# Kernel tuning notes

Hardware: AMD Instinct MI355X
Metric: run time of the kernel (lower is better)

## Reference

```python
import jax, jax.numpy as jnp
import numpy as np

T, N, C, D, S = 512, 32, 1296, 512, 30
NORM_SCALE = 32.0
NEGINF = -1e9


def setup_inputs() -> dict:
    key = jax.random.key(0)
    k1, k2, k3, k4, k5 = jax.random.split(key, 5)
    feats = jax.random.normal(k1, (T * N, D), dtype=jnp.float32)
    classifier_weight = jax.random.normal(k2, (D, C), dtype=jnp.float32)
    labeling = jax.random.randint(k3, (N, S), 1, C)  # targets cannot be blank(0)
    logit_lgts = (T - jax.random.randint(k4, (N,), 0, 32)).astype(jnp.int32)
    labeling_lgts = (S - jax.random.randint(k5, (N,), 0, 5)).astype(jnp.int32)
    return dict(feats=feats, classifier_weight=classifier_weight,
                labeling=labeling, logit_lgts=logit_lgts, labeling_lgts=labeling_lgts)


def _ctc_loss(log_probs, labels, in_lens, lab_lens):
    # log_probs: (T, N, C); labels: (N, S); blank = 0; reduction = 'sum'
    Tt, Nn, Cc = log_probs.shape
    Ss = labels.shape[1]
    L = 2 * Ss + 1
    # extended labeling: blank, l1, blank, l2, ..., blank  -> (N, L)
    ext = jnp.zeros((Nn, L), dtype=labels.dtype).at[:, 1::2].set(labels)
    # gather per-state log-probs: (T, N, L)
    lp_ext = jnp.take_along_axis(log_probs, jnp.broadcast_to(ext[None], (Tt, Nn, L)), axis=2)
    # skip transition s-2 -> s allowed iff s > 1 and ext[s] != ext[s-2]
    skip_ok = jnp.concatenate(
        [jnp.zeros((Nn, 2), dtype=bool), ext[:, 2:] != ext[:, :-2]], axis=1)
    alpha0 = (jnp.full((Nn, L), NEGINF, dtype=log_probs.dtype)
              .at[:, 0].set(lp_ext[0, :, 0])
              .at[:, 1].set(lp_ext[0, :, 1]))

    def step(alpha, inp):
        lp_t, t = inp  # lp_t: (N, L)
        a1 = alpha
        a2 = jnp.pad(alpha[:, :-1], ((0, 0), (1, 0)), constant_values=NEGINF)
        a3 = jnp.where(skip_ok,
                       jnp.pad(alpha[:, :-2], ((0, 0), (2, 0)), constant_values=NEGINF),
                       NEGINF)
        new = jax.nn.logsumexp(jnp.stack([a1, a2, a3], axis=0), axis=0) + lp_t
        # freeze alpha once t reaches a sample's input length
        alpha = jnp.where((t < in_lens)[:, None], new, alpha)
        return alpha, None

    alpha, _ = jax.lax.scan(step, alpha0, (lp_ext[1:], jnp.arange(1, Tt)))
    Ln = 2 * lab_lens + 1  # (N,)
    last = jnp.take_along_axis(alpha, (Ln - 1)[:, None], axis=1)[:, 0]
    last2 = jnp.take_along_axis(alpha, (Ln - 2)[:, None], axis=1)[:, 0]
    nll = -jnp.logaddexp(last, last2)
    return jnp.sum(nll)


def reference(feats, classifier_weight, labeling, logit_lgts, labeling_lgts):
    # RadialCTC: cosine logits with norm_scale, then CTC on log-softmax.
    w_n = classifier_weight / jnp.linalg.norm(classifier_weight, axis=0, keepdims=True)  # (D, C)
    f_n = feats / jnp.linalg.norm(feats, axis=1, keepdims=True)  # (T*N, D)
    logits = NORM_SCALE * (f_n @ w_n)  # (T*N, C)
    log_probs = jax.nn.log_softmax(logits.reshape(T, N, C), axis=-1)
    return _ctc_loss(log_probs, labeling, logit_lgts, labeling_lgts)
```

## Files before the change

### kernel.cpp

```cpp
#include <hip/hip_runtime.h>
#include <stdint.h>
#include <stddef.h>


typedef _Float16 f16;
typedef _Float16 f16x8 __attribute__((ext_vector_type(8)));
typedef float f32x4 __attribute__((ext_vector_type(4)));
typedef __attribute__((address_space(1))) void* as1_void_ptr;
typedef __attribute__((address_space(3))) void* as3_void_ptr;

#define TT 512
#define NN 32
#define CC 1296
#define DD 512
#define SS 30
#define CP 1408
#define LL 61
#define NORM_SCALE 32.0f
#define LOG2E 1.4426950408889634f
#define LN2   0.6931471805599453f

#define PREP_WBLK (CP / 16)
#define PREP_ZBLK 16
#define PREP_FBLK (TT * NN / 4)

#define GEMM_BLK ((TT * NN / 128) * (CP / 128))
#define MEGA_GC  NN
#define MEGA_BLK (MEGA_GC + GEMM_BLK)

__device__ __forceinline__ float fexp2(float x) { return __builtin_amdgcn_exp2f(x); }
__device__ __forceinline__ float flog2(float x) { return __builtin_amdgcn_logf(x); }

__device__ __forceinline__ double dpp_sr1_zero64(double x) {
    long long b = __double_as_longlong(x);
    int lo = (int)(b & 0xFFFFFFFFLL);
    int hi = (int)(b >> 32);
    int lo2 = __builtin_amdgcn_update_dpp(0, lo, 0x138, 0xF, 0xF, false);
    int hi2 = __builtin_amdgcn_update_dpp(0, hi, 0x138, 0xF, 0xF, false);
    return __longlong_as_double(((long long)hi2 << 32) |
                                (unsigned long long)(unsigned int)lo2);
}
__device__ __forceinline__ double dpp_sl1_zero64(double x) {
    long long b = __double_as_longlong(x);
    int lo = (int)(b & 0xFFFFFFFFLL);
    int hi = (int)(b >> 32);
    int lo2 = __builtin_amdgcn_update_dpp(0, lo, 0x130, 0xF, 0xF, false);
    int hi2 = __builtin_amdgcn_update_dpp(0, hi, 0x130, 0xF, 0xF, false);
    return __longlong_as_double(((long long)hi2 << 32) |
                                (unsigned long long)(unsigned int)lo2);
}
template <int CTRL>
__device__ __forceinline__ int dpp_imax_level(int m) {
    int t = __builtin_amdgcn_update_dpp(0, m, CTRL, 0xF, 0xF, false);
    return m > t ? m : t;
}
__device__ __forceinline__ void renorm_d(double& x, int& Mi) {
    int h = (int)(__double_as_longlong(x) >> 32);
    h = dpp_imax_level<0x111>(h);
    h = dpp_imax_level<0x112>(h);
    h = dpp_imax_level<0x114>(h);
    h = dpp_imax_level<0x118>(h);
    int r0 = __builtin_amdgcn_readlane(h, 15);
    int r1 = __builtin_amdgcn_readlane(h, 31);
    int r2 = __builtin_amdgcn_readlane(h, 47);
    int r3 = __builtin_amdgcn_readlane(h, 63);
    int mx = max(max(r0, r1), max(r2, r3));
    int e11 = mx >> 20;
    double scale = __longlong_as_double((long long)(2046 - e11) << 52);
    x *= scale;
    Mi += e11 - 1023;
}

__global__ __launch_bounds__(256) void prep_kernel(const float* __restrict__ W,
                                                   const float* __restrict__ feats,
                                                   f16* __restrict__ wt,
                                                   f16* __restrict__ fn,
                                                   float* __restrict__ sumexp) {
    int bx = blockIdx.x, tid = threadIdx.x;
    if (bx < PREP_WBLK) {
        __shared__ float red[256];
        __shared__ float rqs[16];
        int c0 = bx * 16;
        int cl = tid & 15, dg = tid >> 4;
        int c = c0 + cl;
        float ss = 0.f;
        if (c < CC) {
            for (int d = dg; d < DD; d += 16) {
                float v = W[(size_t)d * CC + c];
                ss += v * v;
            }
        }
        red[tid] = ss;
        __syncthreads();
        if (tid < 16) {
            float s2 = 0.f;
            #pragma unroll
            for (int k = 0; k < 16; ++k) s2 += red[tid + 16 * k];
            rqs[tid] = rsqrtf(s2);
        }
        __syncthreads();
        int c_loc = tid >> 4, dl = tid & 15;
        int cc = c0 + c_loc;
        float rq = rqs[c_loc];
        #pragma unroll 4
        for (int it = 0; it < 32; ++it) {
            int d = dl + it * 16;
            float v = (cc < CC) ? W[(size_t)d * CC + cc] * rq : 0.f;
            wt[(size_t)cc * DD + d] = (f16)v;
        }
    } else if (bx < PREP_WBLK + PREP_ZBLK) {
        int zb = bx - PREP_WBLK;
        float4 z = {0.f, 0.f, 0.f, 0.f};
        ((float4*)sumexp)[zb * 256 + tid] = z;
    } else {
        int fb = bx - PREP_WBLK - PREP_ZBLK;
        int wv = (fb * 256 + tid) >> 6;
        int lane = tid & 63;
        const float4* src = (const float4*)(feats + (size_t)wv * DD) + lane * 2;
        float4 a = src[0], b = src[1];
        float ss = a.x*a.x + a.y*a.y + a.z*a.z + a.w*a.w
                 + b.x*b.x + b.y*b.y + b.z*b.z + b.w*b.w;
        #pragma unroll
        for (int off = 32; off; off >>= 1) ss += __shfl_xor(ss, off);
        float r = rsqrtf(ss);
        f16x8 o;
        o[0]=(f16)(a.x*r); o[1]=(f16)(a.y*r); o[2]=(f16)(a.z*r); o[3]=(f16)(a.w*r);
        o[4]=(f16)(b.x*r); o[5]=(f16)(b.y*r); o[6]=(f16)(b.z*r); o[7]=(f16)(b.w*r);
        *(f16x8*)(fn + (size_t)wv * DD + lane * 8) = o;
    }
}

template <int NT>
__device__ __forceinline__ void gather_chunk(const f16* __restrict__ pb0,
                                             const f16* __restrict__ pb1,
                                             const f16* __restrict__ A,
                                             float* __restrict__ lp_lab,
                                             int n, int c, int rbase, int lane) {
    int lm = lane & 15, hi = lane >> 4;
    const f16* pa0 = A + ((size_t)(c * 128 + rbase + lm) * NN + n) * DD + hi * 8;
    f32x4 acc[NT][2];
    #pragma unroll
    for (int i = 0; i < NT; ++i) {
        acc[i][0] = (f32x4){0.f, 0.f, 0.f, 0.f};
        acc[i][1] = (f32x4){0.f, 0.f, 0.f, 0.f};
    }
    for (int kb = 0; kb < 16; ++kb) {
        f16x8 bf0 = *(const f16x8*)(pb0 + kb * 32);
        f16x8 bf1 = *(const f16x8*)(pb1 + kb * 32);
        #pragma unroll
        for (int i = 0; i < NT; ++i) {
            f16x8 af = *(const f16x8*)(pa0 + (size_t)(i * 16) * NN * DD + kb * 32);
            acc[i][0] = __builtin_amdgcn_mfma_f32_16x16x32_f16(af, bf0, acc[i][0], 0, 0, 0);
            acc[i][1] = __builtin_amdgcn_mfma_f32_16x16x32_f16(af, bf1, acc[i][1], 0, 0, 0);
        }
    }
    #pragma unroll
    for (int i = 0; i < NT; ++i) {
        #pragma unroll
        for (int jn = 0; jn < 2; ++jn) {
            int jc = jn * 16 + lm;
            if (jc >= 31) continue;
            float4 o;
            o.x = acc[i][jn][0] * (NORM_SCALE * LOG2E);
            o.y = acc[i][jn][1] * (NORM_SCALE * LOG2E);
            o.z = acc[i][jn][2] * (NORM_SCALE * LOG2E);
            o.w = acc[i][jn][3] * (NORM_SCALE * LOG2E);
            *(float4*)&lp_lab[((size_t)n * 31 + jc) * TT
                              + c * 128 + rbase + i * 16 + hi * 4] = o;
        }
    }
}

__global__ __launch_bounds__(256) void mega_kernel(const f16* __restrict__ A,
                                                   const f16* __restrict__ B,
                                                   const int* __restrict__ labels,
                                                   const int* __restrict__ in_lens,
                                                   const int* __restrict__ lab_lens,
                                                   float* __restrict__ sumexp,
                                                   float* __restrict__ lp_lab,
                                                   double* __restrict__ part) {
    __shared__ __align__(16) f16 sm[8192];
    int bx = blockIdx.x;
    int tid = threadIdx.x;
    int w = tid >> 6, lane = tid & 63;
    int lm = lane & 15, hi = lane >> 4;
    int sw = (lm >> 1) & 3;

    if (bx >= MEGA_GC) {
        int j = bx - MEGA_GC;
        int x = j & 7, rr = j >> 3;
        int bm = x * 16 + (rr & 15);
        int bn = rr >> 4;
        int wm = w >> 1, wn = w & 1;
        f32x4 acc[4][4];
        f32x4 zero = {0.f, 0.f, 0.f, 0.f};
        #pragma unroll
        for (int i = 0; i < 4; ++i)
            #pragma unroll
            for (int jj = 0; jj < 4; ++jj) acc[i][jj] = zero;

        for (int kb = 0; kb < 16; ++kb) {
            #pragma unroll
            for (int p = 0; p < 2; ++p) {
                int s = p * 256 + tid;
                int row = s >> 2;
                int ch = (s & 3) ^ ((row >> 1) & 3);
                const f16* ga = A + (size_t)(bm * 128 + row) * DD + kb * 32 + ch * 8;
                const f16* gb = B + (size_t)(bn * 128 + row) * DD + kb * 32 + ch * 8;
                __builtin_amdgcn_global_load_lds((as1_void_ptr)ga,
                    (as3_void_ptr)&sm[(p * 256 + w * 64) * 8], 16, 0, 0);
                __builtin_amdgcn_global_load_lds((as1_void_ptr)gb,
                    (as3_void_ptr)&sm[4096 + (p * 256 + w * 64) * 8], 16, 0, 0);
            }
            __syncthreads();
            f16x8 af[4], bf[4];
            #pragma unroll
            for (int i = 0; i < 4; ++i)
                af[i] = *(const f16x8*)&sm[(wm * 64 + i * 16 + lm) * 32 + (hi ^ sw) * 8];
            #pragma unroll
            for (int jj = 0; jj < 4; ++jj)
                bf[jj] = *(const f16x8*)&sm[4096 + (wn * 64 + jj * 16 + lm) * 32 + (hi ^ sw) * 8];
            #pragma unroll
            for (int i = 0; i < 4; ++i)
                #pragma unroll
                for (int jj = 0; jj < 4; ++jj)
                    acc[i][jj] = __builtin_amdgcn_mfma_f32_16x16x32_f16(af[i], bf[jj], acc[i][jj], 0, 0, 0);
            __syncthreads();
        }
        #pragma unroll
        for (int i = 0; i < 4; ++i) {
            float rs[4] = {0.f, 0.f, 0.f, 0.f};
            #pragma unroll
            for (int jj = 0; jj < 4; ++jj) {
                int c = bn * 128 + wn * 64 + jj * 16 + lm;
                bool ok = (c < CC);
                #pragma unroll
                for (int r = 0; r < 4; ++r)
                    rs[r] += ok ? fexp2(acc[i][jj][r] * (NORM_SCALE * LOG2E)) : 0.f;
            }
            #pragma unroll
            for (int off = 1; off < 16; off <<= 1) {
                #pragma unroll
                for (int r = 0; r < 4; ++r) rs[r] += __shfl_xor(rs[r], off);
            }
            if (lm == 0) {
                int rowb = bm * 128 + wm * 64 + i * 16 + hi * 4;
                #pragma unroll
                for (int r = 0; r < 4; ++r) atomicAdd(&sumexp[rowb + r], rs[r]);
            }
        }
        return;
    }

    int n = bx;
    if (w >= 2) {
        __builtin_amdgcn_s_setprio(2);
        int rbase = (w - 2) * 64;
        int cls0 = (lm == 0) ? 0 : labels[n * SS + lm - 1];
        int cls1 = (lm >= 15) ? 0 : labels[n * SS + lm + 15];
        const f16* pb0 = B + (size_t)cls0 * DD + hi * 8;
        const f16* pb1 = B + (size_t)cls1 * DD + hi * 8;
        #pragma unroll 1
        for (int ci = 0; ci < 4; ++ci) {
            int c = (0x2130 >> (ci * 4)) & 3;
            gather_chunk<4>(pb0, pb1, A, lp_lab, n, c, rbase, lane);
            if (ci == 1) __syncthreads();
        }
        __builtin_amdgcn_s_setprio(0);
        __syncthreads();
        __syncthreads();
        return;
    }

    int s = lane;
    bool valid = s < LL;
    int ext = (valid && (s & 1)) ? labels[n * SS + (s >> 1)] : 0;
    int jmap = (valid && (s & 1)) ? ((s >> 1) + 1) : 0;
    int Tin = in_lens[n];
    const float* lpr = lp_lab + ((size_t)n * 31 + jmap) * TT;
    double* vb = (double*)sm;

    if (w == 0) {
        int ext2 = __shfl_up(ext, 2);
        double skipd = ((s >= 2) && valid && (ext != ext2)) ? 1.0 : 0.0;
        double sk1 = dpp_sr1_zero64(skipd);
        double sk2 = dpp_sr1_zero64(sk1);
        double kk2 = skipd * sk2;
        const float4* g4 = (const float4*)lpr;
        double beta = 0.0;
        int Mif = 0;

        auto stepL = [&](float lp) {
            double P = (double)fexp2(lp);
            double b1 = dpp_sr1_zero64(beta);
            double b2 = dpp_sr1_zero64(b1);
            beta = (beta + b1 + b2 * skipd) * P;
        };
        auto step2 = [&](float lp1, float lp2) {
            double q  = (double)fexp2(lp1);
            double P2 = (double)fexp2(lp2);
            double q1 = dpp_sr1_zero64(q);
            double q2 = dpp_sr1_zero64(q1);
            double c1 = q + q1;
            double c2 = fma(skipd, q + q2, q1);
            double c3 = fma(sk1, q1, skipd * q2);
            double c4 = kk2 * q2;
            double b1 = dpp_sr1_zero64(beta);
            double b2 = dpp_sr1_zero64(b1);
            double b3 = dpp_sr1_zero64(b2);
            double b4 = dpp_sr1_zero64(b3);
            double u = fma(c1, b1, q * beta);
            double v2 = fma(c3, b3, c2 * b2);
            beta = (u + fma(c4, b4, v2)) * P2;
        };

        __builtin_amdgcn_s_setprio(3);
        __syncthreads();
        float4 q0 = g4[0];
        beta = (s <= 1) ? (double)fexp2(q0.x) : 0.0;
        stepL(q0.y); stepL(q0.z); stepL(q0.w);
        renorm_d(beta, Mif);
        float4 cu = g4[1];
        for (int gi = 1; gi <= 31; ++gi) {
            float4 nx = g4[gi < 31 ? gi + 1 : 31];
            step2(cu.x, cu.y); step2(cu.z, cu.w);
            if (gi & 1) renorm_d(beta, Mif);
            cu = nx;
        }
        __syncthreads();
        cu = g4[32];
        for (int gi = 32; gi <= 63; ++gi) {
            float4 nx = g4[gi < 63 ? gi + 1 : 63];
            step2(cu.x, cu.y); step2(cu.z, cu.w);
            if (gi & 1) renorm_d(beta, Mif);
            cu = nx;
        }
        renorm_d(beta, Mif);
        __syncthreads();
        __builtin_amdgcn_s_setprio(0);
        double pr = beta * vb[s];
        #pragma unroll
        for (int off = 32; off; off >>= 1) pr += __shfl_xor(pr, off);
        if (s == 0) {
            long long bb = __double_as_longlong(pr);
            int e = (int)(bb >> 52) - 1023;
            double mant = __longlong_as_double((bb & 0xFFFFFFFFFFFFFLL) | (1023LL << 52));
            part[n] = (double)flog2((float)mant) + (double)(e + Mif) + vb[64];
        }
        return;
    }

    {
        float maskf = valid ? 1.f : 0.f;
        int extd2 = __shfl_down(ext, 2);
        double k2d = ((s + 2) < LL && extd2 != ext) ? 1.0 : 0.0;
        int Ln = 2 * lab_lens[n] + 1;
        double v = (s == Ln - 1 || s == Ln - 2) ? 1.0 : 0.0;
        int Mib = 0;

        auto step1b = [&](float lph) {
            float p = maskf * fexp2(lph);
            double u  = (double)p * v;
            double u1 = dpp_sl1_zero64(u);
            double u2 = dpp_sl1_zero64(u1);
            v = fma(k2d, u2, u + u1);
        };

        __builtin_amdgcn_s_setprio(3);
        __syncthreads();
        int tc = Tin - 1;
        int rnc = 0;
        while (tc >= 384) {
            step1b(lpr[tc]);
            if (((++rnc) & 7) == 0) renorm_d(v, Mib);
            --tc;
        }
        renorm_d(v, Mib);
        __syncthreads();
        while (tc >= 256) {
            step1b(lpr[tc]);
            if (((++rnc) & 7) == 0) renorm_d(v, Mib);
            --tc;
        }
        renorm_d(v, Mib);
        vb[s] = v;
        if (s == 0) vb[64] = (double)Mib;
        __builtin_amdgcn_s_setprio(0);
        __syncthreads();
        return;
    }
}

__global__ __launch_bounds__(1024) void final_kernel(const float* __restrict__ sumexp,
                                                     const int* __restrict__ in_lens,
                                                     const double* __restrict__ part,
                                                     float* __restrict__ out) {
    int tid = threadIdx.x;
    int v = tid >> 6, lane = tid & 63;
    __shared__ float nl[NN];
    #pragma unroll
    for (int k = 0; k < 2; ++k) {
        int n = v * 2 + k;
        int Tin = in_lens[n];
        double ms = 0.0;
        for (int t = lane; t < Tin; t += 64)
            ms += (double)flog2(sumexp[(size_t)t * NN + n]);
        #pragma unroll
        for (int off = 32; off; off >>= 1) ms += __shfl_xor(ms, off);
        if (lane == 0) nl[n] = (float)(-(part[n] - ms) * LN2);
    }
    __syncthreads();
    if (tid == 0) {
        float t = 0.f;
        for (int i = 0; i < NN; ++i) t += nl[i];
        out[0] = t;
    }
}

extern "C" void kernel_launch(void* const* d_in, const int* in_sizes, int n_in,
                              void* d_out, int out_size, void* d_ws, size_t ws_size,
                              hipStream_t stream) {
    const float* feats        = (const float*)d_in[0];
    const float* W            = (const float*)d_in[1];
    const int*   labeling     = (const int*)d_in[2];
    const int*   logit_lgts   = (const int*)d_in[3];
    const int*   labeling_lgts= (const int*)d_in[4];
    float* out = (float*)d_out;
    char* ws = (char*)d_ws;

    size_t off = 0;
    f16*   wt     = (f16*)(ws + off);   off += (size_t)CP * DD * 2;
    f16*   fn     = (f16*)(ws + off);   off += (size_t)TT * NN * DD * 2;
    float* sumexp = (float*)(ws + off); off += (size_t)TT * NN * 4;
    float* lp_lab = (float*)(ws + off); off += (size_t)NN * 31 * TT * 4;
    double* part  = (double*)(ws + off); off += NN * 8;

    prep_kernel<<<PREP_WBLK + PREP_ZBLK + PREP_FBLK, 256, 0, stream>>>(
        W, feats, wt, fn, sumexp);
    mega_kernel<<<MEGA_BLK, 256, 0, stream>>>(fn, wt, labeling, logit_lgts,
                                              labeling_lgts, sumexp, lp_lab, part);
    final_kernel<<<1, 1024, 0, stream>>>(sumexp, logit_lgts, part, out);

    (void)in_sizes; (void)n_in; (void)out_size; (void)ws_size;
}
```

Before: 180.2 us.

## Stage label-gather A tiles through LDS and share first chunks across all waves

The per-sample gather GEMM now loads feature rows into per-wave LDS with global_load_lds using XOR swizzled slots, then reads them back for the MFMAs, replacing direct strided global loads. All four waves now compute the first and last time chunks before the CTC recursion starts, and waves 2-3 compute the middle chunks afterwards. Two __syncthreads calls are dropped from the alpha and beta paths to match. This spreads the gather work over more waves and coalesces the loads, at the cost of serial waitcnt stalls with no double buffering and a delay before the recursion waves begin.

```diff
diff --git a/kernel.cpp b/kernel.cpp
--- a/kernel.cpp
+++ b/kernel.cpp
@@ -130,43 +130,56 @@
     }
 }
 
-template <int NT>
-__device__ __forceinline__ void gather_chunk(const f16* __restrict__ pb0,
-                                             const f16* __restrict__ pb1,
-                                             const f16* __restrict__ A,
-                                             float* __restrict__ lp_lab,
-                                             int n, int c, int rbase, int lane) {
+__device__ __forceinline__ void gather_half_lds(f16* sl,
+                                                const f16* __restrict__ pb0,
+                                                const f16* __restrict__ pb1,
+                                                const f16* __restrict__ A,
+                                                float* __restrict__ lp_lab,
+                                                int n, int c, int rbase, int lane) {
     int lm = lane & 15, hi = lane >> 4;
-    const f16* pa0 = A + ((size_t)(c * 128 + rbase + lm) * NN + n) * DD + hi * 8;
-    f32x4 acc[NT][2];
-    #pragma unroll
-    for (int i = 0; i < NT; ++i) {
-        acc[i][0] = (f32x4){0.f, 0.f, 0.f, 0.f};
-        acc[i][1] = (f32x4){0.f, 0.f, 0.f, 0.f};
-    }
-    for (int kb = 0; kb < 16; ++kb) {
-        f16x8 bf0 = *(const f16x8*)(pb0 + kb * 32);
-        f16x8 bf1 = *(const f16x8*)(pb1 + kb * 32);
-        #pragma unroll
-        for (int i = 0; i < NT; ++i) {
-            f16x8 af = *(const f16x8*)(pa0 + (size_t)(i * 16) * NN * DD + kb * 32);
-            acc[i][0] = __builtin_amdgcn_mfma_f32_16x16x32_f16(af, bf0, acc[i][0], 0, 0, 0);
-            acc[i][1] = __builtin_amdgcn_mfma_f32_16x16x32_f16(af, bf1, acc[i][1], 0, 0, 0);
-        }
-    }
-    #pragma unroll
-    for (int i = 0; i < NT; ++i) {
+    int srow = lane >> 4;
+    #pragma unroll 1
+    for (int i = 0; i < 4; ++i) {
+        f32x4 a0 = {0.f, 0.f, 0.f, 0.f};
+        f32x4 a1 = {0.f, 0.f, 0.f, 0.f};
+        int trow0 = c * 128 + rbase + i * 16;
+        #pragma unroll 1
+        for (int q = 0; q < 4; ++q) {
+            asm volatile("s_waitcnt lgkmcnt(0)" ::: "memory");
+            __builtin_amdgcn_sched_barrier(0);
+            #pragma unroll
+            for (int k = 0; k < 4; ++k) {
+                int rloc = k * 4 + srow;
+                int ch = (lane & 15) ^ rloc;
+                const f16* src = A + ((size_t)((trow0 + rloc) * NN + n)) * DD
+                               + q * 128 + ch * 8;
+                __builtin_amdgcn_global_load_lds((as1_void_ptr)src,
+                    (as3_void_ptr)(sl + k * 512), 16, 0, 0);
+            }
+            asm volatile("s_waitcnt vmcnt(0)" ::: "memory");
+            __builtin_amdgcn_sched_barrier(0);
+            #pragma unroll
+            for (int kq = 0; kq < 4; ++kq) {
+                int kb = q * 4 + kq;
+                f16x8 bf0 = *(const f16x8*)(pb0 + kb * 32);
+                f16x8 bf1 = *(const f16x8*)(pb1 + kb * 32);
+                int slot = (kq * 4 + hi) ^ lm;
+                f16x8 af = *(const f16x8*)(sl + lm * 128 + slot * 8);
+                a0 = __builtin_amdgcn_mfma_f32_16x16x32_f16(af, bf0, a0, 0, 0, 0);
+                a1 = __builtin_amdgcn_mfma_f32_16x16x32_f16(af, bf1, a1, 0, 0, 0);
+            }
+        }
         #pragma unroll
         for (int jn = 0; jn < 2; ++jn) {
             int jc = jn * 16 + lm;
             if (jc >= 31) continue;
+            f32x4 av = jn ? a1 : a0;
             float4 o;
-            o.x = acc[i][jn][0] * (NORM_SCALE * LOG2E);
-            o.y = acc[i][jn][1] * (NORM_SCALE * LOG2E);
-            o.z = acc[i][jn][2] * (NORM_SCALE * LOG2E);
-            o.w = acc[i][jn][3] * (NORM_SCALE * LOG2E);
-            *(float4*)&lp_lab[((size_t)n * 31 + jc) * TT
-                              + c * 128 + rbase + i * 16 + hi * 4] = o;
+            o.x = av[0] * (NORM_SCALE * LOG2E);
+            o.y = av[1] * (NORM_SCALE * LOG2E);
+            o.z = av[2] * (NORM_SCALE * LOG2E);
+            o.w = av[3] * (NORM_SCALE * LOG2E);
+            *(float4*)&lp_lab[((size_t)n * 31 + jc) * TT + trow0 + hi * 4] = o;
         }
     }
 }
@@ -253,19 +266,22 @@
     }
 
     int n = bx;
+    int cls0 = (lm == 0) ? 0 : labels[n * SS + lm - 1];
+    int cls1 = (lm >= 15) ? 0 : labels[n * SS + lm + 15];
+    const f16* pb0 = B + (size_t)cls0 * DD + hi * 8;
+    const f16* pb1 = B + (size_t)cls1 * DD + hi * 8;
+    f16* sl = sm + w * 2048;
+
+    __builtin_amdgcn_s_setprio(2);
+    gather_half_lds(sl, pb0, pb1, A, lp_lab, n,
+                    (w < 2) ? 0 : 3, (w & 1) * 64, lane);
+    __builtin_amdgcn_s_setprio(0);
+    __syncthreads();
+
     if (w >= 2) {
         __builtin_amdgcn_s_setprio(2);
-        int rbase = (w - 2) * 64;
-        int cls0 = (lm == 0) ? 0 : labels[n * SS + lm - 1];
-        int cls1 = (lm >= 15) ? 0 : labels[n * SS + lm + 15];
-        const f16* pb0 = B + (size_t)cls0 * DD + hi * 8;
-        const f16* pb1 = B + (size_t)cls1 * DD + hi * 8;
-        #pragma unroll 1
-        for (int ci = 0; ci < 4; ++ci) {
-            int c = (0x2130 >> (ci * 4)) & 3;
-            gather_chunk<4>(pb0, pb1, A, lp_lab, n, c, rbase, lane);
-            if (ci == 1) __syncthreads();
-        }
+        gather_half_lds(sl, pb0, pb1, A, lp_lab, n, 1, (w & 1) * 64, lane);
+        gather_half_lds(sl, pb0, pb1, A, lp_lab, n, 2, (w & 1) * 64, lane);
         __builtin_amdgcn_s_setprio(0);
         __syncthreads();
         __syncthreads();
@@ -315,7 +331,6 @@
         };
 
         __builtin_amdgcn_s_setprio(3);
-        __syncthreads();
         float4 q0 = g4[0];
         beta = (s <= 1) ? (double)fexp2(q0.x) : 0.0;
         stepL(q0.y); stepL(q0.z); stepL(q0.w);
@@ -367,7 +382,6 @@
         };
 
         __builtin_amdgcn_s_setprio(3);
-        __syncthreads();
         int tc = Tin - 1;
         int rnc = 0;
         while (tc >= 384) {
```

Result: no change. 183.3 us (+1.8%).

## Split fused GEMM/gather/CTC mega kernel into separate gather-GEMM and CTC kernels

Applied to the files above, without the earlier changes.

Breaks the single mega kernel, in which gather warps fed CTC recursion warps in the same block through __syncthreads handoffs, into two launches. A gather+GEMM kernel now uses all four waves per gather block (gather_chunk<2>), and a separate 128-thread CTC kernel runs the forward and backward recursions after it finishes. This removes the intra-block pipelining and priority tricks, which simplifies scheduling, but it gives up the overlap between the serial CTC recursion and the GEMM and adds a kernel launch.

```diff
diff --git a/kernel.cpp b/kernel.cpp
--- a/kernel.cpp
+++ b/kernel.cpp
@@ -25,8 +25,8 @@
 #define PREP_FBLK (TT * NN / 4)
 
 #define GEMM_BLK ((TT * NN / 128) * (CP / 128))
-#define MEGA_GC  NN
-#define MEGA_BLK (MEGA_GC + GEMM_BLK)
+#define GG_GATH  NN
+#define GG_BLK   (GG_GATH + GEMM_BLK)
 
 __device__ __forceinline__ float fexp2(float x) { return __builtin_amdgcn_exp2f(x); }
 __device__ __forceinline__ float flog2(float x) { return __builtin_amdgcn_logf(x); }
@@ -171,14 +171,11 @@
     }
 }
 
-__global__ __launch_bounds__(256) void mega_kernel(const f16* __restrict__ A,
-                                                   const f16* __restrict__ B,
-                                                   const int* __restrict__ labels,
-                                                   const int* __restrict__ in_lens,
-                                                   const int* __restrict__ lab_lens,
-                                                   float* __restrict__ sumexp,
-                                                   float* __restrict__ lp_lab,
-                                                   double* __restrict__ part) {
+__global__ __launch_bounds__(256) void gg_kernel(const f16* __restrict__ A,
+                                                 const f16* __restrict__ B,
+                                                 const int* __restrict__ labels,
+                                                 float* __restrict__ sumexp,
+                                                 float* __restrict__ lp_lab) {
     __shared__ __align__(16) f16 sm[8192];
     int bx = blockIdx.x;
     int tid = threadIdx.x;
@@ -186,8 +183,8 @@
     int lm = lane & 15, hi = lane >> 4;
     int sw = (lm >> 1) & 3;
 
-    if (bx >= MEGA_GC) {
-        int j = bx - MEGA_GC;
+    if (bx >= GG_GATH) {
+        int j = bx - GG_GATH;
         int x = j & 7, rr = j >> 3;
         int bm = x * 16 + (rr & 15);
         int bn = rr >> 4;
@@ -253,32 +250,30 @@
     }
 
     int n = bx;
-    if (w >= 2) {
-        __builtin_amdgcn_s_setprio(2);
-        int rbase = (w - 2) * 64;
-        int cls0 = (lm == 0) ? 0 : labels[n * SS + lm - 1];
-        int cls1 = (lm >= 15) ? 0 : labels[n * SS + lm + 15];
-        const f16* pb0 = B + (size_t)cls0 * DD + hi * 8;
-        const f16* pb1 = B + (size_t)cls1 * DD + hi * 8;
-        #pragma unroll 1
-        for (int ci = 0; ci < 4; ++ci) {
-            int c = (0x2130 >> (ci * 4)) & 3;
-            gather_chunk<4>(pb0, pb1, A, lp_lab, n, c, rbase, lane);
-            if (ci == 1) __syncthreads();
-        }
-        __builtin_amdgcn_s_setprio(0);
-        __syncthreads();
-        __syncthreads();
-        return;
-    }
-
-    int s = lane;
+    int rbase = w * 32;
+    int cls0 = (lm == 0) ? 0 : labels[n * SS + lm - 1];
+    int cls1 = (lm >= 15) ? 0 : labels[n * SS + lm + 15];
+    const f16* pb0 = B + (size_t)cls0 * DD + hi * 8;
+    const f16* pb1 = B + (size_t)cls1 * DD + hi * 8;
+    #pragma unroll 1
+    for (int c = 0; c < 4; ++c)
+        gather_chunk<2>(pb0, pb1, A, lp_lab, n, c, rbase, lane);
+}
+
+__global__ __launch_bounds__(128) void ctc_kernel(const float* __restrict__ lp_lab,
+                                                  const int* __restrict__ labels,
+                                                  const int* __restrict__ in_lens,
+                                                  const int* __restrict__ lab_lens,
+                                                  double* __restrict__ part) {
+    __shared__ double vb[65];
+    int n = blockIdx.x;
+    int tid = threadIdx.x;
+    int w = tid >> 6, s = tid & 63;
     bool valid = s < LL;
     int ext = (valid && (s & 1)) ? labels[n * SS + (s >> 1)] : 0;
     int jmap = (valid && (s & 1)) ? ((s >> 1) + 1) : 0;
     int Tin = in_lens[n];
     const float* lpr = lp_lab + ((size_t)n * 31 + jmap) * TT;
-    double* vb = (double*)sm;
 
     if (w == 0) {
         int ext2 = __shfl_up(ext, 2);
@@ -287,16 +282,15 @@
         double sk2 = dpp_sr1_zero64(sk1);
         double kk2 = skipd * sk2;
         const float4* g4 = (const float4*)lpr;
-        double beta = 0.0;
         int Mif = 0;
 
-        auto stepL = [&](float lp) {
+        auto stepL = [&](double& beta, float lp) {
             double P = (double)fexp2(lp);
             double b1 = dpp_sr1_zero64(beta);
             double b2 = dpp_sr1_zero64(b1);
             beta = (beta + b1 + b2 * skipd) * P;
         };
-        auto step2 = [&](float lp1, float lp2) {
+        auto step2 = [&](double& beta, float lp1, float lp2) {
             double q  = (double)fexp2(lp1);
             double P2 = (double)fexp2(lp2);
             double q1 = dpp_sr1_zero64(q);
@@ -314,30 +308,19 @@
             beta = (u + fma(c4, b4, v2)) * P2;
         };
 
-        __builtin_amdgcn_s_setprio(3);
-        __syncthreads();
         float4 q0 = g4[0];
-        beta = (s <= 1) ? (double)fexp2(q0.x) : 0.0;
-        stepL(q0.y); stepL(q0.z); stepL(q0.w);
+        double beta = (s <= 1) ? (double)fexp2(q0.x) : 0.0;
+        stepL(beta, q0.y); stepL(beta, q0.z); stepL(beta, q0.w);
         renorm_d(beta, Mif);
         float4 cu = g4[1];
-        for (int gi = 1; gi <= 31; ++gi) {
-            float4 nx = g4[gi < 31 ? gi + 1 : 31];
-            step2(cu.x, cu.y); step2(cu.z, cu.w);
+        for (int gi = 1; gi <= 63; ++gi) {
+            float4 nx = g4[gi < 63 ? gi + 1 : 63];
+            step2(beta, cu.x, cu.y); step2(beta, cu.z, cu.w);
             if (gi & 1) renorm_d(beta, Mif);
             cu = nx;
         }
-        __syncthreads();
-        cu = g4[32];
-        for (int gi = 32; gi <= 63; ++gi) {
-            float4 nx = g4[gi < 63 ? gi + 1 : 63];
-            step2(cu.x, cu.y); step2(cu.z, cu.w);
-            if (gi & 1) renorm_d(beta, Mif);
-            cu = nx;
-        }
         renorm_d(beta, Mif);
         __syncthreads();
-        __builtin_amdgcn_s_setprio(0);
         double pr = beta * vb[s];
         #pragma unroll
         for (int off = 32; off; off >>= 1) pr += __shfl_xor(pr, off);
@@ -366,17 +349,8 @@
             v = fma(k2d, u2, u + u1);
         };
 
-        __builtin_amdgcn_s_setprio(3);
-        __syncthreads();
         int tc = Tin - 1;
         int rnc = 0;
-        while (tc >= 384) {
-            step1b(lpr[tc]);
-            if (((++rnc) & 7) == 0) renorm_d(v, Mib);
-            --tc;
-        }
-        renorm_d(v, Mib);
-        __syncthreads();
         while (tc >= 256) {
             step1b(lpr[tc]);
             if (((++rnc) & 7) == 0) renorm_d(v, Mib);
@@ -385,7 +359,6 @@
         renorm_d(v, Mib);
         vb[s] = v;
         if (s == 0) vb[64] = (double)Mib;
-        __builtin_amdgcn_s_setprio(0);
         __syncthreads();
         return;
     }
@@ -437,8 +410,9 @@
 
     prep_kernel<<<PREP_WBLK + PREP_ZBLK + PREP_FBLK, 256, 0, stream>>>(
         W, feats, wt, fn, sumexp);
-    mega_kernel<<<MEGA_BLK, 256, 0, stream>>>(fn, wt, labeling, logit_lgts,
-                                              labeling_lgts, sumexp, lp_lab, part);
+    gg_kernel<<<GG_BLK, 256, 0, stream>>>(fn, wt, labeling, sumexp, lp_lab);
+    ctc_kernel<<<NN, 128, 0, stream>>>(lp_lab, labeling, logit_lgts,
+                                       labeling_lgts, part);
     final_kernel<<<1, 1024, 0, stream>>>(sumexp, logit_lgts, part, out);
 
     (void)in_sizes; (void)n_in; (void)out_size; (void)ws_size;
```

Result: no change. 180.8 us (+0.3%).
